# Kernel tuning notes

Hardware: AMD Instinct MI355X
Metric: run time of the kernel (lower is better)

Reference implementation:

```python
import jax, jax.numpy as jnp
import numpy as np

GS_ITERS = 10
GS_TAU = 0.5
NEG = -1e9
B, L, D, H = 4, 512, 64, 128


def gphi_scores(x, W1, b1, W2, b2):
    # Faithful to: concat([x_i, x_j]) -> Linear(2D,H) -> ReLU -> Linear(H,1).squeeze(-1)
    # Linear on the concat of [x_i, x_j] == x_i @ W1[:D] + x_j @ W1[D:] (fused, no [B,L,L,2D] tensor).
    d = x.shape[-1]
    pi = jnp.einsum('bld,dh->blh', x, W1[:d])   # row-index half of concat
    pj = jnp.einsum('bld,dh->blh', x, W1[d:])   # col-index half of concat
    h = jax.nn.relu(pi[:, :, None, :] + pj[:, None, :, :] + b1)  # [B,L,L,H]
    return jnp.einsum('blmh,h->blm', h, W2[:, 0]) + b2[0]        # [B,L,L]


def gumbel_sinkhorn(log_alpha, gumbel, pad_mask, tau, n_iters):
    # (scores + gumbel noise)/tau, mask padded rows/cols, alternate row/col log-normalization.
    la = (log_alpha + gumbel) / tau
    la = jnp.where(pad_mask, NEG, la)

    def step(la, _):
        la = la - jax.nn.logsumexp(la, axis=2, keepdims=True)  # row normalize
        la = la - jax.nn.logsumexp(la, axis=1, keepdims=True)  # col normalize
        la = jnp.where(pad_mask, NEG, la)
        return la, None

    la, _ = jax.lax.scan(step, la, None, length=n_iters)
    return jnp.exp(la)


def make_pad_mask(seq_lens, max_len):
    # mask_map logic: for a sequence of length s, rows < s have cols < s valid; rows >= s fully invalid.
    ar = jnp.arange(max_len)
    s = seq_lens[:, None, None]
    valid = (ar[None, :, None] < s) & (ar[None, None, :] < s)
    return ~valid  # True where gumbel-masked


def setup_inputs() -> dict:
    key = jax.random.key(0)
    ks = jax.random.split(key, 8)
    event_time = jax.random.uniform(ks[0], (B, L), dtype=jnp.float32) * 10.0
    event_type = jax.random.randint(ks[1], (B, L), 0, 50, dtype=jnp.int32)
    clean_enc_out = jax.random.normal(ks[2], (B, L, D), dtype=jnp.float32)
    seq_lens = jax.random.randint(ks[3], (B,), 1, L + 1, dtype=jnp.int32)
    u = jax.random.uniform(ks[4], (B, L, L), dtype=jnp.float32, minval=1e-6, maxval=1.0 - 1e-6)
    gumbel_noise = -jnp.log(-jnp.log(u))
    # gphi_mlp params (xavier-ish scaling)
    W1 = jax.random.normal(ks[5], (2 * D, H), dtype=jnp.float32) * (1.0 / np.sqrt(2 * D))
    b1 = jnp.full((H,), 0.01, dtype=jnp.float32)
    W2 = jax.random.normal(ks[6], (H, 1), dtype=jnp.float32) * (1.0 / np.sqrt(H))
    b2 = jnp.full((1,), 0.01, dtype=jnp.float32)
    return {"event_time": event_time, "event_type": event_type,
            "clean_enc_out": clean_enc_out, "seq_lens": seq_lens,
            "gumbel_noise": gumbel_noise, "W1": W1, "b1": b1, "W2": W2, "b2": b2}


def reference(event_time, event_type, clean_enc_out, seq_lens, gumbel_noise, W1, b1, W2, b2):
    pad_mask = make_pad_mask(seq_lens, event_time.shape[1])
    scores = gphi_scores(clean_enc_out, W1, b1, W2, b2)           # [B,L,L]
    perm = gumbel_sinkhorn(scores, gumbel_noise, pad_mask, GS_TAU, GS_ITERS)
    # same_perm_matrix=True, no_time_noise=True path
    types_permed = jnp.einsum('bl,blm->bm', event_type.astype(jnp.float32), perm)
    times_permed = jnp.einsum('bl,blm->bm', event_time, perm)
    return types_permed, times_permed, perm
```

## Files before the change

### kernel.cpp

```cpp
#include <hip/hip_runtime.h>
#include <cstdint>

#define BB 4
#define LL 512
#define DD 64
#define HH 128
#define NEGV -1000000000.0f
#define NBLK 256
#define NTHR 1024
#define NACT 64

union U8 { unsigned long long u; float2 f; };

__device__ __forceinline__ float2 cload_f2(const float* p) {
    U8 v;
    v.u = __hip_atomic_load((const unsigned long long*)p,
                            __ATOMIC_RELAXED, __HIP_MEMORY_SCOPE_AGENT);
    return v.f;
}
__device__ __forceinline__ void cstore_f2(float* p, float2 x) {
    U8 v; v.f = x;
    __hip_atomic_store((unsigned long long*)p, v.u,
                       __ATOMIC_RELAXED, __HIP_MEMORY_SCOPE_AGENT);
}

__device__ __forceinline__ void grid_barrier(unsigned* cnt, unsigned target) {
    __builtin_amdgcn_fence(__ATOMIC_RELEASE, "workgroup");
    __syncthreads();
    if (threadIdx.x == 0) {
        __hip_atomic_fetch_add(cnt, 1u, __ATOMIC_RELAXED, __HIP_MEMORY_SCOPE_AGENT);
        while (__hip_atomic_load(cnt, __ATOMIC_RELAXED, __HIP_MEMORY_SCOPE_AGENT) < target) {}
    }
    __builtin_amdgcn_fence(__ATOMIC_ACQUIRE, "workgroup");
    __syncthreads();
}

__device__ __forceinline__ float hmax4(float4 v) {
    return fmaxf(fmaxf(v.x, v.y), fmaxf(v.z, v.w));
}

__global__ __launch_bounds__(NTHR, 4) void mega(
    const float* __restrict__ etime, const int* __restrict__ etype,
    const float* __restrict__ x, const int* __restrict__ slens,
    const float* __restrict__ gum, const float* __restrict__ W1,
    const float* __restrict__ b1, const float* __restrict__ W2,
    const float* __restrict__ b2, float* __restrict__ out, float* __restrict__ ws)
{
    __shared__ float smem[24704];

    unsigned* cntA = (unsigned*)ws;
    float* laG   = ws + 256;
    float* cpkG  = laG + (size_t)BB * LL * LL;
    float* poutG = cpkG + (size_t)2 * BB * 16 * LL * 2;

    const int t = threadIdx.x;
    const int bx = blockIdx.x;

    {
        float* sp  = smem;
        float* sq  = smem + 8192;
        float* sx  = smem + 16384;
        float* sw2 = smem + 24576;
        int jt = bx & 7, it8 = (bx >> 3) & 7, b = bx >> 6;
        int i0 = it8 << 6, j0 = jt << 6;

        #pragma unroll
        for (int k = 0; k < 2; ++k) {
            int u = (k << 10) + t;
            int tile = u >> 10;
            int v = u & 1023;
            int row = v >> 4, q4 = v & 15;
            const float* src = x + (size_t)(b * LL + (tile ? j0 : i0) + row) * DD + (q4 << 2);
            *(float4*)(sx + ((tile << 6) + row) * DD + (q4 << 2)) = *(const float4*)src;
        }
        if (t < HH) sw2[t] = W2[t];
        __syncthreads();

        #pragma unroll
        for (int o = 0; o < 4; ++o) {
            int u = (o << 10) + t;
            int arr = u >> 11;
            int v = u & 2047;
            int row = v >> 5, hq = v & 31;
            const float* wb = W1 + (size_t)(arr * DD) * HH + (hq << 2);
            float4 acc;
            if (arr == 0) acc = *(const float4*)(b1 + (hq << 2));
            else          acc = make_float4(0.f, 0.f, 0.f, 0.f);
            const float* xr = sx + ((arr << 6) + row) * DD;
            #pragma unroll 8
            for (int d = 0; d < DD; ++d) {
                float xv = xr[d];
                float4 w = *(const float4*)(wb + d * HH);
                acc.x = fmaf(xv, w.x, acc.x); acc.y = fmaf(xv, w.y, acc.y);
                acc.z = fmaf(xv, w.z, acc.z); acc.w = fmaf(xv, w.w, acc.w);
            }
            int dq = hq ^ ((row >> 2) & 7);
            *(float4*)((arr ? sq : sp) + row * HH + (dq << 2)) = acc;
        }
        __syncthreads();

        int hg = t >> 8, tt = t & 255;
        int w = tt >> 6, lane = tt & 63;
        int ti = ((w >> 1) << 3) + (lane >> 3);
        int tj = ((w & 1) << 3) + (lane & 7);
        int kti = ti & 7, ktj = tj & 7;

        float acc[4][4];
        #pragma unroll
        for (int a = 0; a < 4; ++a)
            #pragma unroll
            for (int c = 0; c < 4; ++c) acc[a][c] = 0.f;

        for (int hq = hg * 8; hq < hg * 8 + 8; ++hq) {
            float4 w4 = *(const float4*)(sw2 + (hq << 2));
            int offi = (hq ^ kti) << 2;
            int offj = (hq ^ ktj) << 2;
            float4 pa[4], pb[4];
            #pragma unroll
            for (int a = 0; a < 4; ++a) pa[a] = *(const float4*)(sp + (4*ti + a) * HH + offi);
            #pragma unroll
            for (int c = 0; c < 4; ++c) pb[c] = *(const float4*)(sq + (4*tj + c) * HH + offj);
            #pragma unroll
            for (int a = 0; a < 4; ++a) {
                #pragma unroll
                for (int c = 0; c < 4; ++c) {
                    float t0 = fmaxf(pa[a].x + pb[c].x, 0.f);
                    float t1 = fmaxf(pa[a].y + pb[c].y, 0.f);
                    float t2 = fmaxf(pa[a].z + pb[c].z, 0.f);
                    float t3 = fmaxf(pa[a].w + pb[c].w, 0.f);
                    float s = acc[a][c];
                    s += t0 * w4.x; s += t1 * w4.y; s += t2 * w4.z; s += t3 * w4.w;
                    acc[a][c] = s;
                }
            }
        }
        __syncthreads();
        float* cbuf = smem;
        #pragma unroll
        for (int a = 0; a < 4; ++a)
            #pragma unroll
            for (int c = 0; c < 4; ++c)
                cbuf[(((hg << 8) + tt) << 4) + (a << 2) + c] = acc[a][c];
        __syncthreads();

        int tt2 = t >> 2, a2 = t & 3;
        int w2_ = tt2 >> 6, lane2 = tt2 & 63;
        int ti2 = ((w2_ >> 1) << 3) + (lane2 >> 3);
        int tj2 = ((w2_ & 1) << 3) + (lane2 & 7);
        float4 o = make_float4(0.f, 0.f, 0.f, 0.f);
        #pragma unroll
        for (int g = 0; g < 4; ++g) {
            float4 pp = *(const float4*)(cbuf + (((g << 8) + tt2) << 4) + (a2 << 2));
            o.x += pp.x; o.y += pp.y; o.z += pp.z; o.w += pp.w;
        }
        int sl = slens[b];
        float bb2 = b2[0];
        int ig = i0 + 4 * ti2 + a2;
        int jb = j0 + 4 * tj2;
        float4 g4 = *(const float4*)(gum + ((size_t)(b * LL + ig)) * LL + jb);
        bool iv = ig < sl;
        float4 res;
        res.x = (iv && (jb + 0) < sl) ? (o.x + bb2 + g4.x) * 2.0f : NEGV;
        res.y = (iv && (jb + 1) < sl) ? (o.y + bb2 + g4.y) * 2.0f : NEGV;
        res.z = (iv && (jb + 2) < sl) ? (o.z + bb2 + g4.z) * 2.0f : NEGV;
        res.w = (iv && (jb + 3) < sl) ? (o.w + bb2 + g4.w) * 2.0f : NEGV;
        float* lap = laG + ((size_t)(b * LL + ig)) * LL + jb;
        cstore_f2(lap,     make_float2(res.x, res.y));
        cstore_f2(lap + 2, make_float2(res.z, res.w));
    }
    grid_barrier(cntA, NBLK);

    if (bx >= NACT) return;

    const int b2i = bx >> 4;
    const int stripe = bx & 15;
    const int r0 = stripe << 5;
    unsigned* cntB = (unsigned*)ws + 32 + (b2i << 5);
    float* sla  = smem;
    float* redm = smem + 16384;
    float* reds = smem + 17408;
    float* clse = smem + 18432;
    const int sl_a = slens[b2i];
    float tyv = 0.f, tmv = 0.f;

    {
        const float* src = laG + (((size_t)(b2i << 9) + r0) << 9);
        #pragma unroll
        for (int k = 0; k < 8; ++k) {
            int u = (k << 10) + t;
            float2 v = cload_f2(src + (u << 1));
            *(float2*)(sla + (u << 1)) = v;
        }
        if (t < 512) clse[t] = 0.f;
        __syncthreads();
    }

    for (int it = 0; it < 10; ++it) {
        const int par = it & 1;
        const int last = (it == 9);
        {
            int r = t >> 5, cq = t & 31;
            int grow = r0 + r;
            bool ivR = grow < sl_a;
            float4 v[4];
            #pragma unroll
            for (int k = 0; k < 4; ++k) {
                int cb = (cq + (k << 5)) << 2;
                float4 a = *(float4*)(sla + (r << 9) + cb);
                float4 l = *(const float4*)(clse + cb);
                v[k].x = (ivR && (cb + 0) < sl_a) ? a.x - l.x : NEGV;
                v[k].y = (ivR && (cb + 1) < sl_a) ? a.y - l.y : NEGV;
                v[k].z = (ivR && (cb + 2) < sl_a) ? a.z - l.z : NEGV;
                v[k].w = (ivR && (cb + 3) < sl_a) ? a.w - l.w : NEGV;
            }
            float m = fmaxf(fmaxf(hmax4(v[0]), hmax4(v[1])), fmaxf(hmax4(v[2]), hmax4(v[3])));
            #pragma unroll
            for (int off = 16; off; off >>= 1) m = fmaxf(m, __shfl_xor(m, off));
            float s = 0.f;
            #pragma unroll
            for (int k = 0; k < 4; ++k)
                s += __expf(v[k].x - m) + __expf(v[k].y - m) + __expf(v[k].z - m) + __expf(v[k].w - m);
            #pragma unroll
            for (int off = 16; off; off >>= 1) s += __shfl_xor(s, off);
            float lse = m + __logf(s);
            #pragma unroll
            for (int k = 0; k < 4; ++k) {
                v[k].x -= lse; v[k].y -= lse; v[k].z -= lse; v[k].w -= lse;
                *(float4*)(sla + (r << 9) + ((cq + (k << 5)) << 2)) = v[k];
            }
            __syncthreads();

            int c = t & 511, half = t >> 9;
            float vv[16];
            #pragma unroll
            for (int rr = 0; rr < 16; ++rr) vv[rr] = sla[(((half << 4) + rr) << 9) + c];
            float mp = vv[0];
            #pragma unroll
            for (int rr = 1; rr < 16; ++rr) mp = fmaxf(mp, vv[rr]);
            float spv = 0.f;
            #pragma unroll
            for (int rr = 0; rr < 16; ++rr) spv += __expf(vv[rr] - mp);
            redm[(half << 9) + c] = mp;
            reds[(half << 9) + c] = spv;
            __syncthreads();
            if (half == 0) {
                float m1 = redm[512 + c], s1 = reds[512 + c];
                float M = fmaxf(mp, m1);
                float S = fmaf(spv, __expf(mp - M), s1 * __expf(m1 - M));
                cstore_f2(cpkG + (size_t)(((((par * BB) + b2i) << 4) + stripe) * LL + c) * 2,
                          make_float2(M, S));
            }
        }
        grid_barrier(cntB, (it + 1) * 16);
        {
            if (t < 512) {
                const float* pB = cpkG + (size_t)((((par * BB) + b2i) << 4) * LL) * 2;
                float mreg[16], sreg[16];
                #pragma unroll
                for (int g = 0; g < 16; ++g) {
                    float2 ms = cload_f2(pB + (size_t)(g * LL + t) * 2);
                    mreg[g] = ms.x; sreg[g] = ms.y;
                }
                float M = mreg[0];
                #pragma unroll
                for (int g = 1; g < 16; ++g) M = fmaxf(M, mreg[g]);
                float S = 0.f;
                #pragma unroll
                for (int g = 0; g < 16; ++g)
                    S = fmaf(sreg[g], __expf(mreg[g] - M), S);
                clse[t] = M + __logf(S);
            }
            __syncthreads();

            if (last) {
                int r = t >> 5, cq = t & 31;
                int grow = r0 + r;
                bool ivR = grow < sl_a;
                float etf = (float)etype[(b2i << 9) + grow];
                float etv = etime[(b2i << 9) + grow];
                float4 p[4];
                #pragma unroll
                for (int k = 0; k < 4; ++k) {
                    int cb = (cq + (k << 5)) << 2;
                    float4 v = *(float4*)(sla + (r << 9) + cb);
                    float4 l = *(const float4*)(clse + cb);
                    float4 q;
                    q.x = (ivR && (cb + 0) < sl_a) ? __expf(v.x - l.x) : 0.f;
                    q.y = (ivR && (cb + 1) < sl_a) ? __expf(v.y - l.y) : 0.f;
                    q.z = (ivR && (cb + 2) < sl_a) ? __expf(v.z - l.z) : 0.f;
                    q.w = (ivR && (cb + 3) < sl_a) ? __expf(v.w - l.w) : 0.f;
                    p[k] = q;
                    *(float4*)(out + 2 * BB * LL + (((size_t)(b2i << 9) + grow) << 9) + cb) = q;
                }
                #pragma unroll
                for (int k = 0; k < 4; ++k) {
                    int cb = (cq + (k << 5)) << 2;
                    *(float4*)(sla + (r << 9) + cb) =
                        make_float4(p[k].x * etf, p[k].y * etf, p[k].z * etf, p[k].w * etf);
                }
                __syncthreads();
                {
                    int c2 = t & 511, h2 = t >> 9;
                    float sA = 0.f;
                    #pragma unroll
                    for (int rr = 0; rr < 16; ++rr) sA += sla[(((h2 << 4) + rr) << 9) + c2];
                    redm[(h2 << 9) + c2] = sA;
                }
                __syncthreads();
                if (t < 512) tyv = redm[t] + redm[512 + t];
                __syncthreads();
                #pragma unroll
                for (int k = 0; k < 4; ++k) {
                    int cb = (cq + (k << 5)) << 2;
                    *(float4*)(sla + (r << 9) + cb) =
                        make_float4(p[k].x * etv, p[k].y * etv, p[k].z * etv, p[k].w * etv);
                }
                __syncthreads();
                {
                    int c2 = t & 511, h2 = t >> 9;
                    float sB = 0.f;
                    #pragma unroll
                    for (int rr = 0; rr < 16; ++rr) sB += sla[(((h2 << 4) + rr) << 9) + c2];
                    reds[(h2 << 9) + c2] = sB;
                }
                __syncthreads();
                if (t < 512) {
                    tmv = reds[t] + reds[512 + t];
                    cstore_f2(poutG + (size_t)(((b2i << 4) + stripe) * LL + t) * 2,
                              make_float2(tyv, tmv));
                }
            }
        }
    }
    grid_barrier(cntB, 11 * 16);

    if (t < 32) {
        int c = (stripe << 5) + t;
        float a = 0.f, d = 0.f;
        #pragma unroll
        for (int s = 0; s < 16; ++s) {
            float2 p = cload_f2(poutG + (size_t)(((b2i << 4) + s) * LL + c) * 2);
            a += p.x; d += p.y;
        }
        out[(b2i << 9) + c] = a;
        out[BB * LL + (b2i << 9) + c] = d;
    }
}

extern "C" void kernel_launch(void* const* d_in, const int* in_sizes, int n_in,
                              void* d_out, int out_size, void* d_ws, size_t ws_size,
                              hipStream_t stream)
{
    const float* etime = (const float*)d_in[0];
    const int*   etype = (const int*)d_in[1];
    const float* x     = (const float*)d_in[2];
    const int*   slens = (const int*)d_in[3];
    const float* gum   = (const float*)d_in[4];
    const float* W1    = (const float*)d_in[5];
    const float* b1    = (const float*)d_in[6];
    const float* W2    = (const float*)d_in[7];
    const float* b2    = (const float*)d_in[8];
    float* out = (float*)d_out;
    float* wsf = (float*)d_ws;

    hipMemsetAsync(d_ws, 0, 1024, stream);

    void* args[] = {(void*)&etime, (void*)&etype, (void*)&x, (void*)&slens, (void*)&gum,
                    (void*)&W1, (void*)&b1, (void*)&W2, (void*)&b2, (void*)&out, (void*)&wsf};
    hipError_t err = hipLaunchCooperativeKernel((const void*)mega, dim3(NBLK), dim3(NTHR),
                                                args, 0, stream);
    if (err != hipSuccess) {
        mega<<<NBLK, NTHR, 0, stream>>>(etime, etype, x, slens, gum, W1, b1, W2, b2, out, wsf);
    }
}
```

Baseline: 126.3 us.

## Replace grid barriers with per-tile flags and precompute projections once globally

Each block now computes its 8 rows of the x@W1 projections once and writes them to global memory. Before this, every 64x64 tile block recomputed its 64+64 row projections. The counting grid barriers are replaced with per-producer flags, so tile blocks wait only on the GEMV rows they need and Sinkhorn stripes wait only on their tiles and peer stripes. This removes redundant GEMV work and lets blocks start without a full grid barrier, at the cost of an extra global round trip for the projections and more memset of the flag area.

```diff
diff --git a/kernel.cpp b/kernel.cpp
--- a/kernel.cpp
+++ b/kernel.cpp
@@ -24,20 +24,21 @@
                        __ATOMIC_RELAXED, __HIP_MEMORY_SCOPE_AGENT);
 }
 
-__device__ __forceinline__ void grid_barrier(unsigned* cnt, unsigned target) {
-    __builtin_amdgcn_fence(__ATOMIC_RELEASE, "workgroup");
-    __syncthreads();
-    if (threadIdx.x == 0) {
-        __hip_atomic_fetch_add(cnt, 1u, __ATOMIC_RELAXED, __HIP_MEMORY_SCOPE_AGENT);
-        while (__hip_atomic_load(cnt, __ATOMIC_RELAXED, __HIP_MEMORY_SCOPE_AGENT) < target) {}
-    }
-    __builtin_amdgcn_fence(__ATOMIC_ACQUIRE, "workgroup");
-    __syncthreads();
+__device__ __forceinline__ void set_flag(unsigned* f) {
+    __hip_atomic_store(f, 1u, __ATOMIC_RELAXED, __HIP_MEMORY_SCOPE_AGENT);
+}
+__device__ __forceinline__ void wait_flag(unsigned* f) {
+    while (__hip_atomic_load(f, __ATOMIC_RELAXED, __HIP_MEMORY_SCOPE_AGENT) == 0u) {}
 }
 
 __device__ __forceinline__ float hmax4(float4 v) {
     return fmaxf(fmaxf(v.x, v.y), fmaxf(v.z, v.w));
 }
+
+#define FLG_GEMV 0
+#define FLG_TILE 256
+#define FLG_ITER 512
+#define FLG_POUT 1152
 
 __global__ __launch_bounds__(NTHR, 4) void mega(
     const float* __restrict__ etime, const int* __restrict__ etype,
@@ -46,56 +47,68 @@
     const float* __restrict__ b1, const float* __restrict__ W2,
     const float* __restrict__ b2, float* __restrict__ out, float* __restrict__ ws)
 {
-    __shared__ float smem[24704];
-
-    unsigned* cntA = (unsigned*)ws;
-    float* laG   = ws + 256;
+    __shared__ float smem[19072];
+
+    unsigned* flg = (unsigned*)ws;
+    float* piG   = ws + 2048;
+    float* pjG   = piG + BB * LL * HH;
+    float* laG   = pjG + BB * LL * HH;
     float* cpkG  = laG + (size_t)BB * LL * LL;
     float* poutG = cpkG + (size_t)2 * BB * 16 * LL * 2;
 
     const int t = threadIdx.x;
     const int bx = blockIdx.x;
+
+    {
+        int arr = t >> 9;
+        int row = (t >> 6) & 7;
+        int h0  = (t & 63) << 1;
+        int grow = (bx << 3) + row;
+        const float* xr = x + (size_t)grow * DD;
+        const float* wb = W1 + (size_t)(arr * DD) * HH + h0;
+        float a0 = arr ? 0.f : b1[h0];
+        float a1 = arr ? 0.f : b1[h0 + 1];
+        #pragma unroll 8
+        for (int d = 0; d < DD; ++d) {
+            float xv = xr[d];
+            float2 w = *(const float2*)(wb + d * HH);
+            a0 = fmaf(xv, w.x, a0);
+            a1 = fmaf(xv, w.y, a1);
+        }
+        cstore_f2((arr ? pjG : piG) + (size_t)grow * HH + h0, make_float2(a0, a1));
+        __builtin_amdgcn_fence(__ATOMIC_RELEASE, "workgroup");
+        __syncthreads();
+        if (t == 0) set_flag(flg + FLG_GEMV + bx);
+    }
 
     {
         float* sp  = smem;
         float* sq  = smem + 8192;
-        float* sx  = smem + 16384;
-        float* sw2 = smem + 24576;
+        float* sw2 = smem + 18944;
         int jt = bx & 7, it8 = (bx >> 3) & 7, b = bx >> 6;
         int i0 = it8 << 6, j0 = jt << 6;
-
-        #pragma unroll
-        for (int k = 0; k < 2; ++k) {
-            int u = (k << 10) + t;
-            int tile = u >> 10;
-            int v = u & 1023;
-            int row = v >> 4, q4 = v & 15;
-            const float* src = x + (size_t)(b * LL + (tile ? j0 : i0) + row) * DD + (q4 << 2);
-            *(float4*)(sx + ((tile << 6) + row) * DD + (q4 << 2)) = *(const float4*)src;
-        }
+        int rowb = b * LL + i0, colb = b * LL + j0;
+
+        if (t < 8)              wait_flag(flg + FLG_GEMV + (b << 6) + (it8 << 3) + t);
+        else if (t < 16)        wait_flag(flg + FLG_GEMV + (b << 6) + (jt << 3) + (t - 8));
         if (t < HH) sw2[t] = W2[t];
         __syncthreads();
 
         #pragma unroll
-        for (int o = 0; o < 4; ++o) {
-            int u = (o << 10) + t;
-            int arr = u >> 11;
-            int v = u & 2047;
-            int row = v >> 5, hq = v & 31;
-            const float* wb = W1 + (size_t)(arr * DD) * HH + (hq << 2);
-            float4 acc;
-            if (arr == 0) acc = *(const float4*)(b1 + (hq << 2));
-            else          acc = make_float4(0.f, 0.f, 0.f, 0.f);
-            const float* xr = sx + ((arr << 6) + row) * DD;
-            #pragma unroll 8
-            for (int d = 0; d < DD; ++d) {
-                float xv = xr[d];
-                float4 w = *(const float4*)(wb + d * HH);
-                acc.x = fmaf(xv, w.x, acc.x); acc.y = fmaf(xv, w.y, acc.y);
-                acc.z = fmaf(xv, w.z, acc.z); acc.w = fmaf(xv, w.w, acc.w);
-            }
-            int dq = hq ^ ((row >> 2) & 7);
-            *(float4*)((arr ? sq : sp) + row * HH + (dq << 2)) = acc;
+        for (int k = 0; k < 8; ++k) {
+            int idx = (k << 10) + t;
+            int buf = idx >> 12;
+            int u   = idx & 4095;
+            int row = u >> 6;
+            int du  = u & 63;
+            int q   = du >> 1;
+            int hi  = du & 1;
+            int dq  = q ^ ((row >> 2) & 7);
+            const float* src = (buf ? pjG + (size_t)(colb + row) * HH
+                                    : piG + (size_t)(rowb + row) * HH) + (du << 1);
+            float2 v = cload_f2(src);
+            float* dst = (buf ? sq : sp) + row * HH + (dq << 2) + (hi << 1);
+            *(float2*)dst = v;
         }
         __syncthreads();
 
@@ -167,15 +180,16 @@
         float* lap = laG + ((size_t)(b * LL + ig)) * LL + jb;
         cstore_f2(lap,     make_float2(res.x, res.y));
         cstore_f2(lap + 2, make_float2(res.z, res.w));
-    }
-    grid_barrier(cntA, NBLK);
+        __builtin_amdgcn_fence(__ATOMIC_RELEASE, "workgroup");
+        __syncthreads();
+        if (t == 0) set_flag(flg + FLG_TILE + (b << 6) + (it8 << 3) + jt);
+    }
 
     if (bx >= NACT) return;
 
     const int b2i = bx >> 4;
     const int stripe = bx & 15;
     const int r0 = stripe << 5;
-    unsigned* cntB = (unsigned*)ws + 32 + (b2i << 5);
     float* sla  = smem;
     float* redm = smem + 16384;
     float* reds = smem + 17408;
@@ -184,6 +198,8 @@
     float tyv = 0.f, tmv = 0.f;
 
     {
+        if (t < 8) wait_flag(flg + FLG_TILE + (b2i << 6) + ((stripe >> 1) << 3) + t);
+        __syncthreads();
         const float* src = laG + (((size_t)(b2i << 9) + r0) << 9);
         #pragma unroll
         for (int k = 0; k < 8; ++k) {
@@ -250,8 +266,12 @@
                 cstore_f2(cpkG + (size_t)(((((par * BB) + b2i) << 4) + stripe) * LL + c) * 2,
                           make_float2(M, S));
             }
-        }
-        grid_barrier(cntB, (it + 1) * 16);
+            __builtin_amdgcn_fence(__ATOMIC_RELEASE, "workgroup");
+            __syncthreads();
+            if (t == 0) set_flag(flg + FLG_ITER + (((b2i * 10) + it) << 4) + stripe);
+            if (t < 16) wait_flag(flg + FLG_ITER + (((b2i * 10) + it) << 4) + t);
+            __syncthreads();
+        }
         {
             if (t < 512) {
                 const float* pB = cpkG + (size_t)((((par * BB) + b2i) << 4) * LL) * 2;
@@ -329,11 +349,15 @@
                     cstore_f2(poutG + (size_t)(((b2i << 4) + stripe) * LL + t) * 2,
                               make_float2(tyv, tmv));
                 }
-            }
-        }
-    }
-    grid_barrier(cntB, 11 * 16);
-
+                __builtin_amdgcn_fence(__ATOMIC_RELEASE, "workgroup");
+                __syncthreads();
+                if (t == 0) set_flag(flg + FLG_POUT + (b2i << 4) + stripe);
+            }
+        }
+    }
+
+    if (t < 16) wait_flag(flg + FLG_POUT + (b2i << 4) + t);
+    __syncthreads();
     if (t < 32) {
         int c = (stripe << 5) + t;
         float a = 0.f, d = 0.f;
@@ -363,7 +387,7 @@
     float* out = (float*)d_out;
     float* wsf = (float*)d_ws;
 
-    hipMemsetAsync(d_ws, 0, 1024, stream);
+    hipMemsetAsync(d_ws, 0, 8192, stream);
 
     void* args[] = {(void*)&etime, (void*)&etype, (void*)&x, (void*)&slens, (void*)&gum,
                     (void*)&W1, (void*)&b1, (void*)&W2, (void*)&b2, (void*)&out, (void*)&wsf};
```

Result: faster. 112.8 us (-10.6%).
